# Kernel tuning notes

Hardware: AMD Instinct MI355X
Metric: run time of the kernel (lower is better)

Reference implementation:

```python
import jax, jax.numpy as jnp
import numpy as np

STEP = 3
INTERVAL = STEP // 2          # 1
W_LEN = 2 * INTERVAL + 1      # sliding window length = 3
N_TOK = 2 * STEP + 1          # tokens per position (reg + window + diff) = 7


def setup_inputs() -> dict:
    key = jax.random.key(0)
    k1, k2, k3, k4 = jax.random.split(key, 4)
    b, n, d, r = 8, 1024, 1024, 256
    x = jax.random.normal(k1, (b, n, d), dtype=jnp.float32)
    mask = jnp.ones((b, N_TOK, 1), dtype=jnp.float32)
    # nn.Linear(input_dim, red_dim, bias=False) weight: (red_dim, input_dim)
    W = jax.random.normal(k2, (r, d), dtype=jnp.float32) / np.sqrt(d).astype(np.float32)
    pos_local = jax.random.normal(k3, (1, N_TOK, r), dtype=jnp.float32)
    reg_token = jax.random.normal(k4, (1, 1, r), dtype=jnp.float32)
    pad_tokens = jnp.zeros((1, INTERVAL, d), dtype=jnp.float32)
    return {"x": x, "mask": mask, "W": W, "pos_local": pos_local,
            "reg_token": reg_token, "pad_tokens": pad_tokens}


def reference(x, mask, W, pos_local, reg_token, pad_tokens):
    # Faithful, vectorized version of the 'local' branch (dropout in eval mode).
    b, n, d = x.shape
    r = W.shape[0]
    pad = jnp.broadcast_to(pad_tokens, (b, INTERVAL, d))
    xp = jnp.concatenate([pad, x, pad], axis=1)            # (b, n + 2*INTERVAL, d)
    # torch loop runs i in [INTERVAL, n): m computed positions; first INTERVAL rows of x_ stay zero
    m = n - INTERVAL
    idx = jnp.arange(m)[:, None] + jnp.arange(W_LEN)[None, :]   # (m, W_LEN), window starts at i-INTERVAL
    wins = xp[:, idx]                                        # (b, m, W_LEN, d)
    center = wins[:, :, INTERVAL][:, :, None, :]             # (b, m, 1, d)
    x_new = jnp.concatenate([wins, wins - center], axis=2)   # (b, m, 2*W_LEN, d)
    y = jnp.einsum('bmwd,rd->bmwr', x_new, W)                # reduce_embedding, no bias
    reg = jnp.broadcast_to(reg_token.reshape(1, 1, 1, r), (b, m, 1, r))
    out = (jnp.concatenate([reg, y], axis=2) + pos_local[None]) * mask[:, None]  # (b, m, N_TOK, r)
    # first INTERVAL sequence positions were never written (remain zero)
    out = jnp.concatenate([jnp.zeros((b, INTERVAL, N_TOK, r), out.dtype), out], axis=1)
    return out
```

## Files before the change

### kernel.cpp

```cpp
#include <hip/hip_runtime.h>

#define BB 8
#define NN 1024
#define DD 1024
#define RR 256
#define MM (BB * NN)
#define NTOK 7

typedef __bf16 bf16x8 __attribute__((ext_vector_type(8)));
typedef float f32x4 __attribute__((ext_vector_type(4)));

__global__ __launch_bounds__(256) void wcvt(const float* __restrict__ W, __bf16* __restrict__ Wb) {
  const int i = (blockIdx.x * 256 + threadIdx.x) * 4;
  float4 v = *reinterpret_cast<const float4*>(W + i);
  union { __bf16 b[4]; ushort4 u; } p;
  p.b[0] = (__bf16)v.x; p.b[1] = (__bf16)v.y; p.b[2] = (__bf16)v.z; p.b[3] = (__bf16)v.w;
  *reinterpret_cast<ushort4*>(Wb + i) = p.u;
}

__global__ void pad_proj(const float* __restrict__ Wt, const float* __restrict__ pad,
                         float* __restrict__ Ppad) {
  const int c = blockIdx.x;
  const int lane = threadIdx.x;
  float s = 0.f;
  for (int k = lane; k < DD; k += 64) s += Wt[(size_t)c * DD + k] * pad[k];
#pragma unroll
  for (int off = 32; off; off >>= 1) s += __shfl_down(s, off);
  if (lane == 0) Ppad[c] = s;
}

__device__ __forceinline__ bf16x8 cvt8(const float4& lo, const float4& hi) {
  bf16x8 r;
  r[0] = (__bf16)lo.x; r[1] = (__bf16)lo.y; r[2] = (__bf16)lo.z; r[3] = (__bf16)lo.w;
  r[4] = (__bf16)hi.x; r[5] = (__bf16)hi.y; r[6] = (__bf16)hi.z; r[7] = (__bf16)hi.w;
  return r;
}

__global__ __launch_bounds__(256) void gemm_fused(const float* __restrict__ X,
                                                  const __bf16* __restrict__ Wb,
                                                  const float* __restrict__ Ppad,
                                                  const float* __restrict__ mask,
                                                  const float* __restrict__ pos,
                                                  const float* __restrict__ regtok,
                                                  float* __restrict__ Phalo,
                                                  float* __restrict__ out) {
  const int tid = threadIdx.x;
  const int wave = tid >> 6;
  const int lane = tid & 63;
  const int m0 = blockIdx.x * 16;
  const int c0 = wave * 64;
  const int lr = lane & 15;
  const int lg = lane >> 4;

  const float*  xb = X  + (size_t)(m0 + lr) * DD + lg * 8;
  const __bf16* wb = Wb + (size_t)(c0 + lr) * DD + lg * 8;

  f32x4 acc[4] = {};
  float4 aA[2], aB[2];
  bf16x8 bA[4], bB[4];

#define LD_A(dst, kk) do {                                          \
    dst[0] = *reinterpret_cast<const float4*>(xb + (kk));           \
    dst[1] = *reinterpret_cast<const float4*>(xb + (kk) + 4);       \
  } while (0)
#define LD_B(dst, kk) do {                                          \
    dst[0] = *reinterpret_cast<const bf16x8*>(wb + (kk));           \
    dst[1] = *reinterpret_cast<const bf16x8*>(wb + 16 * DD + (kk)); \
    dst[2] = *reinterpret_cast<const bf16x8*>(wb + 32 * DD + (kk)); \
    dst[3] = *reinterpret_cast<const bf16x8*>(wb + 48 * DD + (kk)); \
  } while (0)
#define MFMA_STEP(aS, bS) do {                                      \
    bf16x8 af = cvt8(aS[0], aS[1]);                                 \
    acc[0] = __builtin_amdgcn_mfma_f32_16x16x32_bf16(af, bS[0], acc[0], 0, 0, 0); \
    acc[1] = __builtin_amdgcn_mfma_f32_16x16x32_bf16(af, bS[1], acc[1], 0, 0, 0); \
    acc[2] = __builtin_amdgcn_mfma_f32_16x16x32_bf16(af, bS[2], acc[2], 0, 0, 0); \
    acc[3] = __builtin_amdgcn_mfma_f32_16x16x32_bf16(af, bS[3], acc[3], 0, 0, 0); \
  } while (0)

  LD_A(aA, 0); LD_B(bA, 0);
  for (int k0 = 0; k0 < DD - 64; k0 += 64) {
    LD_A(aB, k0 + 32); LD_B(bB, k0 + 32);
    MFMA_STEP(aA, bA);
    LD_A(aA, k0 + 64); LD_B(bA, k0 + 64);
    MFMA_STEP(aB, bB);
  }
  LD_A(aB, DD - 32); LD_B(bB, DD - 32);
  MFMA_STEP(aA, bA);
  MFMA_STEP(aB, bB);

#undef LD_A
#undef LD_B
#undef MFMA_STEP

  __shared__ float Pt[16][260];
#pragma unroll
  for (int ni = 0; ni < 4; ++ni)
#pragma unroll
    for (int r = 0; r < 4; ++r)
      Pt[lg * 4 + r][c0 + ni * 16 + lr] = acc[ni][r];
  __syncthreads();

  const int c4 = (tid & 63) * 4;

  {
    const int hr = tid >> 6;
    const int row = (hr < 2) ? hr : hr + 12;
    float4 v = *reinterpret_cast<const float4*>(&Pt[row][c4]);
    *reinterpret_cast<float4*>(&Phalo[(size_t)(m0 + row) * RR + c4]) = v;
  }

  const int b  = m0 >> 10;
  const int n0 = m0 & (NN - 1);

  float mk[NTOK];
#pragma unroll
  for (int t = 0; t < NTOK; ++t) mk[t] = mask[b * NTOK + t];
  const float4 rg = *reinterpret_cast<const float4*>(regtok + c4);
  float4 psv[NTOK];
#pragma unroll
  for (int t = 0; t < NTOK; ++t)
    psv[t] = *reinterpret_cast<const float4*>(pos + (size_t)t * RR + c4);

  const int jlo = (n0 == 0) ? 0 : n0 + 2;
  for (int j = jlo + wave; j < n0 + 16; j += 4) {
    float* outp = out + (((size_t)b * NN + j) * NTOK) * RR + c4;
    if (j == 0) {
      float4 z = make_float4(0.f, 0.f, 0.f, 0.f);
#pragma unroll
      for (int t = 0; t < NTOK; ++t)
        *reinterpret_cast<float4*>(outp + (size_t)t * RR) = z;
      continue;
    }
    float4 q[3];
#pragma unroll
    for (int w = 0; w < 3; ++w) {
      const int src = j - 2 + w;
      q[w] = (src < 0) ? *reinterpret_cast<const float4*>(Ppad + c4)
                       : *reinterpret_cast<const float4*>(&Pt[src - n0][c4]);
    }
#pragma unroll
    for (int t = 0; t < NTOK; ++t) {
      float4 v;
      if (t == 0) {
        v = rg;
      } else if (t <= 3) {
        v = q[t - 1];
      } else {
        const int w = t - 4;
        v = make_float4(q[w].x - q[1].x, q[w].y - q[1].y, q[w].z - q[1].z, q[w].w - q[1].w);
      }
      v.x = (v.x + psv[t].x) * mk[t];
      v.y = (v.y + psv[t].y) * mk[t];
      v.z = (v.z + psv[t].z) * mk[t];
      v.w = (v.w + psv[t].w) * mk[t];
      *reinterpret_cast<float4*>(outp + (size_t)t * RR) = v;
    }
  }
}

#define NCLEAN_ROWS (BB * 126)
__global__ __launch_bounds__(256) void cleanup(const float* __restrict__ Phalo,
                                               const float* __restrict__ mask,
                                               const float* __restrict__ pos,
                                               const float* __restrict__ regtok,
                                               float* __restrict__ out) {
  const int gid = blockIdx.x * 256 + threadIdx.x;
  const int rowIdx = gid >> 6;
  if (rowIdx >= NCLEAN_ROWS) return;
  const int b  = rowIdx / 126;
  const int rr = rowIdx - b * 126;
  const int j  = 16 * ((rr >> 1) + 1) + (rr & 1);
  const int c4 = (gid & 63) * 4;

  float4 q[3];
#pragma unroll
  for (int w = 0; w < 3; ++w)
    q[w] = *reinterpret_cast<const float4*>(&Phalo[((size_t)b * NN + j - 2 + w) * RR + c4]);

  const float4 rg = *reinterpret_cast<const float4*>(regtok + c4);
  float* outp = out + (((size_t)b * NN + j) * NTOK) * RR + c4;

#pragma unroll
  for (int t = 0; t < NTOK; ++t) {
    const float4 ps = *reinterpret_cast<const float4*>(pos + (size_t)t * RR + c4);
    const float m = mask[b * NTOK + t];
    float4 v;
    if (t == 0) {
      v = rg;
    } else if (t <= 3) {
      v = q[t - 1];
    } else {
      const int w = t - 4;
      v = make_float4(q[w].x - q[1].x, q[w].y - q[1].y, q[w].z - q[1].z, q[w].w - q[1].w);
    }
    v.x = (v.x + ps.x) * m;
    v.y = (v.y + ps.y) * m;
    v.z = (v.z + ps.z) * m;
    v.w = (v.w + ps.w) * m;
    *reinterpret_cast<float4*>(outp + (size_t)t * RR) = v;
  }
}

extern "C" void kernel_launch(void* const* d_in, const int* in_sizes, int n_in,
                              void* d_out, int out_size, void* d_ws, size_t ws_size,
                              hipStream_t stream) {
  const float* x      = (const float*)d_in[0];
  const float* mask   = (const float*)d_in[1];
  const float* W      = (const float*)d_in[2];
  const float* pos    = (const float*)d_in[3];
  const float* regtok = (const float*)d_in[4];
  const float* pad    = (const float*)d_in[5];
  float* out = (float*)d_out;

  float*  Phalo = (float*)d_ws;
  __bf16* Wb    = (__bf16*)((char*)d_ws + (size_t)MM * RR * 4);
  float*  Ppad  = (float*)((char*)d_ws + (size_t)MM * RR * 4 + (size_t)RR * DD * 2);

  wcvt<<<RR * DD / (256 * 4), 256, 0, stream>>>(W, Wb);
  pad_proj<<<RR, 64, 0, stream>>>(W, pad, Ppad);
  gemm_fused<<<MM / 16, 256, 0, stream>>>(x, Wb, Ppad, mask, pos, regtok, Phalo, out);
  cleanup<<<NCLEAN_ROWS * 64 / 256, 256, 0, stream>>>(Phalo, mask, pos, regtok, out);
}
```

Measured before the change: 148.0 us.

## Stage X tiles in LDS via direct global-to-LDS loads shared across waves

Before, each of the four waves loaded the same 16-row X slice from global memory into registers. Now the block stages each 16x64 fp32 tile of X once into double-buffered, XOR-swizzled LDS using global_load_lds, and all waves read their fragments from LDS. The intent is to cut redundant global and L2 traffic for X by four times. In exchange it adds a block-wide barrier on every k-step. W loads are no longer software-prefetched and are issued each iteration right before use.

```diff
diff --git a/kernel.cpp b/kernel.cpp
--- a/kernel.cpp
+++ b/kernel.cpp
@@ -6,6 +6,8 @@
 #define RR 256
 #define MM (BB * NN)
 #define NTOK 7
+#define BKT 64
+#define NKT (DD / BKT)
 
 typedef __bf16 bf16x8 __attribute__((ext_vector_type(8)));
 typedef float f32x4 __attribute__((ext_vector_type(4)));
@@ -52,47 +54,57 @@
   const int lr = lane & 15;
   const int lg = lane >> 4;
 
-  const float*  xb = X  + (size_t)(m0 + lr) * DD + lg * 8;
+  __shared__ __align__(16) float Ab[2][16 * BKT];
+  __shared__ float Pt[16][260];
+
+  const int srow = tid >> 4;
+  const int sgc  = (tid & 15) ^ (srow & 7);
+  const float* srcbase = X + (size_t)(m0 + srow) * DD + sgc * 4;
+  float* dst0 = &Ab[0][wave * 256];
+  float* dst1 = &Ab[1][wave * 256];
+
+  const int g00 = lr * 16 + lg * 2;
+  const int p00 = g00 ^ (lr & 7);
+  const int p10 = (g00 + 8) ^ (lr & 7);
+
   const __bf16* wb = Wb + (size_t)(c0 + lr) * DD + lg * 8;
 
   f32x4 acc[4] = {};
-  float4 aA[2], aB[2];
-  bf16x8 bA[4], bB[4];
-
-#define LD_A(dst, kk) do {                                          \
-    dst[0] = *reinterpret_cast<const float4*>(xb + (kk));           \
-    dst[1] = *reinterpret_cast<const float4*>(xb + (kk) + 4);       \
-  } while (0)
-#define LD_B(dst, kk) do {                                          \
-    dst[0] = *reinterpret_cast<const bf16x8*>(wb + (kk));           \
-    dst[1] = *reinterpret_cast<const bf16x8*>(wb + 16 * DD + (kk)); \
-    dst[2] = *reinterpret_cast<const bf16x8*>(wb + 32 * DD + (kk)); \
-    dst[3] = *reinterpret_cast<const bf16x8*>(wb + 48 * DD + (kk)); \
-  } while (0)
-#define MFMA_STEP(aS, bS) do {                                      \
-    bf16x8 af = cvt8(aS[0], aS[1]);                                 \
-    acc[0] = __builtin_amdgcn_mfma_f32_16x16x32_bf16(af, bS[0], acc[0], 0, 0, 0); \
-    acc[1] = __builtin_amdgcn_mfma_f32_16x16x32_bf16(af, bS[1], acc[1], 0, 0, 0); \
-    acc[2] = __builtin_amdgcn_mfma_f32_16x16x32_bf16(af, bS[2], acc[2], 0, 0, 0); \
-    acc[3] = __builtin_amdgcn_mfma_f32_16x16x32_bf16(af, bS[3], acc[3], 0, 0, 0); \
-  } while (0)
-
-  LD_A(aA, 0); LD_B(bA, 0);
-  for (int k0 = 0; k0 < DD - 64; k0 += 64) {
-    LD_A(aB, k0 + 32); LD_B(bB, k0 + 32);
-    MFMA_STEP(aA, bA);
-    LD_A(aA, k0 + 64); LD_B(bA, k0 + 64);
-    MFMA_STEP(aB, bB);
-  }
-  LD_A(aB, DD - 32); LD_B(bB, DD - 32);
-  MFMA_STEP(aA, bA);
-  MFMA_STEP(aB, bB);
-
-#undef LD_A
-#undef LD_B
-#undef MFMA_STEP
-
-  __shared__ float Pt[16][260];
+
+#define STAGE(dst, kt) \
+  __builtin_amdgcn_global_load_lds( \
+      (const __attribute__((address_space(1))) void*)(srcbase + (kt) * BKT), \
+      (__attribute__((address_space(3))) void*)(dst), 16, 0, 0)
+
+  STAGE(dst0, 0);
+  __syncthreads();
+
+  for (int kt = 0; kt < NKT; ++kt) {
+    const int cur = kt & 1;
+    if (kt < NKT - 1) {
+      STAGE((cur ? dst0 : dst1), kt + 1);
+    }
+    bf16x8 bfr[4][2];
+#pragma unroll
+    for (int ni = 0; ni < 4; ++ni) {
+#pragma unroll
+      for (int ks = 0; ks < 2; ++ks)
+        bfr[ni][ks] = *reinterpret_cast<const bf16x8*>(wb + (size_t)ni * 16 * DD + kt * BKT + ks * 32);
+    }
+    const float4* ab4 = reinterpret_cast<const float4*>(&Ab[cur][0]);
+    float4 lo0 = ab4[p00], hi0 = ab4[p00 ^ 1];
+    float4 lo1 = ab4[p10], hi1 = ab4[p10 ^ 1];
+    bf16x8 af0 = cvt8(lo0, hi0);
+    bf16x8 af1 = cvt8(lo1, hi1);
+#pragma unroll
+    for (int ni = 0; ni < 4; ++ni) {
+      acc[ni] = __builtin_amdgcn_mfma_f32_16x16x32_bf16(af0, bfr[ni][0], acc[ni], 0, 0, 0);
+      acc[ni] = __builtin_amdgcn_mfma_f32_16x16x32_bf16(af1, bfr[ni][1], acc[ni], 0, 0, 0);
+    }
+    __syncthreads();
+  }
+#undef STAGE
+
 #pragma unroll
   for (int ni = 0; ni < 4; ++ni)
 #pragma unroll
```

Result: faster. 133.4 us (-9.9%).
